# Optimization experiments

Measured on AMD Instinct MI355X. Metric: run time of the kernel, lower is better.

The kernel has to match this reference:

```python
import jax, jax.numpy as jnp
import numpy as np

N = 60000      # total atoms
E = 120000     # total directed bond edges
B = 1024       # molecules per batch
DIN = 88       # unpacked node feature bits
DE = 32        # unpacked edge feature bits
EMB = 256      # graph_dims
L = 4          # num MPNN layers
HID = 512      # attention hid_dim
H = 8          # n_heads
HD = HID // H  # head dim


def _bn(x, g, b):
    # BatchNorm1d in training mode: biased batch stats over dim 0
    m = x.mean(0)
    v = x.var(0)
    return g * (x - m) * jax.lax.rsqrt(v + 1e-5) + b


def setup_inputs() -> dict:
    ks = jax.random.split(jax.random.key(0), 24)
    p = lambda i, s: jax.random.normal(ks[i], s, jnp.float32) * 0.02
    z = lambda s: jnp.zeros(s, jnp.float32)
    o = lambda s: jnp.ones(s, jnp.float32)
    return {
        "x": jax.random.uniform(ks[0], (N, DIN), jnp.float32),
        "edge_index": jax.random.randint(ks[1], (2, E), 0, N),
        "edge_attr": jax.random.uniform(ks[2], (E, DE), jnp.float32),
        "batch": jnp.sort(jax.random.randint(ks[3], (N,), 0, B)),
        "fp": jax.random.uniform(ks[4], (B, 2048), jnp.float32),
        "target": (jax.random.uniform(ks[5], (B, 3)) > 0.5).astype(jnp.float32),
        "lin_w": p(6, (DIN, EMB)), "lin_b": z(EMB),
        "msg_w1": p(7, (L, 2 * EMB + DE, EMB)), "msg_b1": z((L, EMB)), "msg_g1": o((L, EMB)), "msg_be1": z((L, EMB)),
        "msg_w2": p(8, (L, EMB, EMB)), "msg_b2": z((L, EMB)), "msg_g2": o((L, EMB)), "msg_be2": z((L, EMB)),
        "upd_w1": p(9, (L, 2 * EMB, EMB)), "upd_b1": z((L, EMB)), "upd_g1": o((L, EMB)), "upd_be1": z((L, EMB)),
        "upd_w2": p(10, (L, EMB, EMB)), "upd_b2": z((L, EMB)), "upd_g2": o((L, EMB)), "upd_be2": z((L, EMB)),
        "gl_w1": p(11, (EMB, 1024)), "gl_b1": z(1024),
        "gl_w2": p(12, (1024, 1024)), "gl_b2": z(1024),
        "gl_w3": p(13, (1024, HID)), "gl_b3": z(HID),
        "fp_w": p(14, (2048, HID)), "fp_b": z(HID),
        "att_w": p(15, (2, 4, HID, HID)), "att_b": z((2, 4, HID)),
        "bind_w": p(16, (HID, 3)), "bind_b": z(3),
    }


def reference(x, edge_index, edge_attr, batch, fp, target,
              lin_w, lin_b,
              msg_w1, msg_b1, msg_g1, msg_be1, msg_w2, msg_b2, msg_g2, msg_be2,
              upd_w1, upd_b1, upd_g1, upd_be1, upd_w2, upd_b2, upd_g2, upd_be2,
              gl_w1, gl_b1, gl_w2, gl_b2, gl_w3, gl_b3,
              fp_w, fp_b, att_w, att_b, bind_w, bind_b):
    relu = jax.nn.relu
    src, dst = edge_index[0], edge_index[1]  # PyG: row 0 = source j, row 1 = target i
    h = x @ lin_w + lin_b  # (n, EMB)
    for l in range(msg_w1.shape[0]):
        # message: gather dst/src node feats + edge feats -> 2-layer BN MLP
        m = jnp.concatenate([h[dst], h[src], edge_attr], axis=-1)  # (e, 2*EMB+DE)
        m = relu(_bn(m @ msg_w1[l] + msg_b1[l], msg_g1[l], msg_be1[l]))
        m = relu(_bn(m @ msg_w2[l] + msg_b2[l], msg_g2[l], msg_be2[l]))
        # aggregate: scatter-add into destination nodes
        aggr = jax.ops.segment_sum(m, dst, num_segments=h.shape[0])  # (n, EMB)
        # update: concat with h -> 2-layer BN MLP; residual from MPNNModel
        u = jnp.concatenate([h, aggr], axis=-1)
        u = relu(_bn(u @ upd_w1[l] + upd_b1[l], upd_g1[l], upd_be1[l]))
        u = relu(_bn(u @ upd_w2[l] + upd_b2[l], upd_g2[l], upd_be2[l]))
        h = h + u
    # global mean pool per graph
    nb = fp.shape[0]
    sums = jax.ops.segment_sum(h, batch, num_segments=nb)
    cnt = jax.ops.segment_sum(jnp.ones((h.shape[0],), h.dtype), batch, num_segments=nb)
    g = sums / jnp.maximum(cnt, 1.0)[:, None]  # (B, EMB)
    # graph MLP (dropout = identity at inference)
    g = relu(g @ gl_w1 + gl_b1)
    g = relu(g @ gl_w2 + gl_b2)
    g = g @ gl_w3 + gl_b3  # (B, 512)
    fpf = relu(fp @ fp_w + fp_b)  # (B, 512)

    def attn(i, q, k, v):
        Q = (q @ att_w[i, 0] + att_b[i, 0]).reshape(-1, H, HD)
        K = (k @ att_w[i, 1] + att_b[i, 1]).reshape(-1, H, HD)
        V = (v @ att_w[i, 2] + att_b[i, 2]).reshape(-1, H, HD)
        # energy[b,h,d,e] = Q[b,h,d]*K[b,h,e] / sqrt(HD): outer product per head
        energy = jnp.einsum('bhd,bhe->bhde', Q, K) / jnp.sqrt(jnp.float32(HD))
        a = jax.nn.softmax(energy, axis=-1)
        o = jnp.einsum('bhde,bhe->bhd', a, V)
        # torch permute(0,2,1,3).view: flatten in (head_dim, head) order
        o = o.transpose(0, 2, 1).reshape(-1, H * HD)
        return o @ att_w[i, 3] + att_b[i, 3]

    g = g + attn(0, fpf, g, g)   # cross attention fp -> graph
    g = attn(1, g, g, g)          # self attention
    bind = g @ bind_w + bind_b    # (B, 3)
    # stable BCE-with-logits, mean reduction
    loss = jnp.mean(jnp.maximum(bind, 0.0) - bind * target + jnp.log1p(jnp.exp(-jnp.abs(bind))))
    return loss, jax.nn.sigmoid(bind)
```

## Files before the change

kernel.cpp:

```cpp
#include <hip/hip_runtime.h>
#include <hip/hip_bf16.h>
#include <math.h>

typedef long long i64;
typedef __hip_bfloat16 bf16;
typedef __attribute__((ext_vector_type(8))) short bfx8;
typedef __attribute__((ext_vector_type(4))) float f32x4;

#define NATOMS 60000
#define NEDGES 120000
#define NB     1024
#define EMB    256
#define NL     4
#define HIDF   512
#define NH     8
#define HD     64

__device__ __forceinline__ void storeT(float* p, float v) { *p = v; }
__device__ __forceinline__ void storeT(bf16* p, float v) { *p = __float2bfloat16(v); }

__device__ __forceinline__ void gl_lds16(const void* g, void* l) {
  __builtin_amdgcn_global_load_lds((const __attribute__((address_space(1))) void*)g,
                                   (__attribute__((address_space(3))) void*)l, 16, 0, 0);
}

template<int MODE, typename TO>
__global__ __launch_bounds__(256, 2) void mgemm_k(
    const bf16* __restrict__ A, const bf16* __restrict__ A2,
    const int* __restrict__ gdst, const int* __restrict__ gsrc,
    const bf16* __restrict__ Wt,
    const float* __restrict__ bias, const float* __restrict__ resid,
    TO* __restrict__ C, float* __restrict__ stats,
    int M, int Kp, int N, int doRelu)
{
  __shared__ short As[128 * 64];
  __shared__ short Bs[128 * 64];
  __shared__ float sSum[128], sSq[128];

  const int tid = threadIdx.x;
  const int w = tid >> 6, lane = tid & 63;
  const int wr = w >> 1, wc = w & 1;
  const int row0 = blockIdx.y * 128, col0 = blockIdx.x * 128;

  int rI[4], slotG[4], dIdx[4], sIdx[4], rClamp[4];
  #pragma unroll
  for (int i = 0; i < 4; ++i) {
    int lin = i * 256 + tid;
    int r = lin >> 3, sl = lin & 7;
    rI[i] = r;
    slotG[i] = sl ^ (r & 7);
    rClamp[i] = min(row0 + r, M - 1);
    if (MODE == 1) { dIdx[i] = gdst[rClamp[i]]; sIdx[i] = gsrc[rClamp[i]]; }
  }

  f32x4 acc[4][4];
  #pragma unroll
  for (int a = 0; a < 4; ++a)
    #pragma unroll
    for (int b = 0; b < 4; ++b)
      acc[a][b] = (f32x4){0.f, 0.f, 0.f, 0.f};

  const int KT = Kp >> 6;
  for (int kt = 0; kt < KT; ++kt) {
    const int k0 = kt << 6;
    #pragma unroll
    for (int i = 0; i < 4; ++i) {
      const bf16* g;
      int ko = slotG[i] * 8;
      if constexpr (MODE == 0) {
        g = A + (i64)rClamp[i] * Kp + k0 + ko;
      } else if constexpr (MODE == 1) {
        if (k0 < 256)      g = A  + (i64)dIdx[i] * EMB + k0 + ko;
        else if (k0 < 512) g = A  + (i64)sIdx[i] * EMB + (k0 - 256) + ko;
        else               g = A2 + (i64)rClamp[i] * 64 + (k0 - 512) + ko;
      } else {
        g = (k0 < 256) ? A  + (i64)rClamp[i] * EMB + k0 + ko
                       : A2 + (i64)rClamp[i] * EMB + (k0 - 256) + ko;
      }
      gl_lds16(g, (char*)&As[0] + i * 4096 + w * 1024);
    }
    #pragma unroll
    for (int i = 0; i < 4; ++i) {
      const bf16* g = Wt + (i64)(col0 + rI[i]) * Kp + k0 + slotG[i] * 8;
      gl_lds16(g, (char*)&Bs[0] + i * 4096 + w * 1024);
    }
    __syncthreads();

    #pragma unroll
    for (int ks = 0; ks < 2; ++ks) {
      bfx8 af[4], bf_[4];
      #pragma unroll
      for (int mi = 0; mi < 4; ++mi) {
        int r = wr * 64 + mi * 16 + (lane & 15);
        int q = ks * 4 + (lane >> 4);
        int s = q ^ (r & 7);
        af[mi] = *(const bfx8*)&As[r * 64 + s * 8];
      }
      #pragma unroll
      for (int ni = 0; ni < 4; ++ni) {
        int n = wc * 64 + ni * 16 + (lane & 15);
        int q = ks * 4 + (lane >> 4);
        int s = q ^ (n & 7);
        bf_[ni] = *(const bfx8*)&Bs[n * 64 + s * 8];
      }
      #pragma unroll
      for (int mi = 0; mi < 4; ++mi)
        #pragma unroll
        for (int ni = 0; ni < 4; ++ni)
          acc[mi][ni] = __builtin_amdgcn_mfma_f32_16x16x32_bf16(af[mi], bf_[ni], acc[mi][ni], 0, 0, 0);
    }
    __syncthreads();
  }

  #pragma unroll
  for (int mi = 0; mi < 4; ++mi) {
    #pragma unroll
    for (int j = 0; j < 4; ++j) {
      int row = row0 + wr * 64 + mi * 16 + (lane >> 4) * 4 + j;
      if (row < M) {
        #pragma unroll
        for (int ni = 0; ni < 4; ++ni) {
          int col = col0 + wc * 64 + ni * 16 + (lane & 15);
          float v = acc[mi][ni][j];
          if (bias)  v += bias[col];
          if (resid) v += resid[(i64)row * N + col];
          if (doRelu) v = fmaxf(v, 0.f);
          storeT(&C[(i64)row * N + col], v);
        }
      }
    }
  }

  if (stats) {
    if (tid < 128) { sSum[tid] = 0.f; sSq[tid] = 0.f; }
    __syncthreads();
    #pragma unroll
    for (int ni = 0; ni < 4; ++ni) {
      float ps = 0.f, pq = 0.f;
      #pragma unroll
      for (int mi = 0; mi < 4; ++mi)
        #pragma unroll
        for (int j = 0; j < 4; ++j) {
          int row = row0 + wr * 64 + mi * 16 + (lane >> 4) * 4 + j;
          if (row < M) { float v = acc[mi][ni][j]; ps += v; pq += v * v; }
        }
      ps += __shfl_xor(ps, 16); ps += __shfl_xor(ps, 32);
      pq += __shfl_xor(pq, 16); pq += __shfl_xor(pq, 32);
      if (lane < 16) {
        int c = wc * 64 + ni * 16 + lane;
        atomicAdd(&sSum[c], ps); atomicAdd(&sSq[c], pq);
      }
    }
    __syncthreads();
    if (tid < 128) {
      atomicAdd(&stats[col0 + tid], sSum[tid]);
      atomicAdd(&stats[256 + col0 + tid], sSq[tid]);
    }
  }
}

struct WDesc { const float* W; bf16* Wt; int K, N, Kp, bStart; };
struct WPack { WDesc d[29]; int cnt; };

__global__ __launch_bounds__(256) void wcvt_k(WPack p) {
  int bid = blockIdx.x;
  int di = 0;
  for (int i = 1; i < 29; ++i) if (i < p.cnt && bid >= p.d[i].bStart) di = i;
  WDesc wd = p.d[di];
  int t = bid - wd.bStart;
  int tilesN = wd.N >> 5;
  int tn = t % tilesN, tk = t / tilesN;
  __shared__ float tl[32][33];
  int tx = threadIdx.x & 31, ty = threadIdx.x >> 5;
  #pragma unroll
  for (int ii = 0; ii < 4; ++ii) {
    int k = tk * 32 + ty + ii * 8;
    int n = tn * 32 + tx;
    tl[ty + ii * 8][tx] = (k < wd.K) ? wd.W[(i64)k * wd.N + n] : 0.f;
  }
  __syncthreads();
  #pragma unroll
  for (int ii = 0; ii < 4; ++ii) {
    int n = tn * 32 + ty + ii * 8;
    int k = tk * 32 + tx;
    wd.Wt[(i64)n * wd.Kp + k] = __float2bfloat16(tl[tx][ty + ii * 8]);
  }
}

__global__ void padcvt_k(const float* __restrict__ S, bf16* __restrict__ D,
                         int rows, int sc, int dc) {
  i64 total = (i64)rows * dc;
  for (i64 i = (i64)blockIdx.x * blockDim.x + threadIdx.x; i < total;
       i += (i64)gridDim.x * blockDim.x) {
    int r = (int)(i / dc), c = (int)(i % dc);
    D[i] = __float2bfloat16(c < sc ? S[(i64)r * sc + c] : 0.f);
  }
}

__global__ void cvt_k(const float* __restrict__ S, bf16* __restrict__ D, i64 total) {
  i64 i0 = ((i64)blockIdx.x * blockDim.x + threadIdx.x) * 4;
  i64 stride = (i64)gridDim.x * blockDim.x * 4;
  for (i64 i = i0; i < total; i += stride) {
    float4 v = *(const float4*)(S + i);
    D[i + 0] = __float2bfloat16(v.x);
    D[i + 1] = __float2bfloat16(v.y);
    D[i + 2] = __float2bfloat16(v.z);
    D[i + 3] = __float2bfloat16(v.w);
  }
}

template<int HASADD>
__global__ __launch_bounds__(256) void bnap_k(
    const bf16* __restrict__ X, const bf16* __restrict__ addIn, bf16* __restrict__ Y,
    const float* __restrict__ st, const float* __restrict__ gam, const float* __restrict__ bet,
    i64 total, float invM)
{
  __shared__ float sc[256], sh[256];
  {
    int c = threadIdx.x;
    float mean = st[c] * invM;
    float var  = st[256 + c] * invM - mean * mean;
    float rs   = rsqrtf(var + 1e-5f);
    float s    = gam[c] * rs;
    sc[c] = s; sh[c] = bet[c] - mean * s;
  }
  __syncthreads();
  i64 i0 = ((i64)blockIdx.x * blockDim.x + threadIdx.x) * 8;
  i64 stride = (i64)gridDim.x * blockDim.x * 8;
  for (i64 i = i0; i < total; i += stride) {
    bfx8 xv = *(const bfx8*)((const short*)X + i);
    bfx8 av;
    if (HASADD) av = *(const bfx8*)((const short*)addIn + i);
    int c0 = (int)(i & 255);
    bfx8 o;
    #pragma unroll
    for (int j = 0; j < 8; ++j) {
      unsigned short u = (unsigned short)xv[j];
      float x = __bfloat162float(*reinterpret_cast<const bf16*>(&u));
      int c = c0 + j;
      float t = fmaxf(x * sc[c] + sh[c], 0.f);
      if (HASADD) {
        unsigned short ua = (unsigned short)av[j];
        t += __bfloat162float(*reinterpret_cast<const bf16*>(&ua));
      }
      bf16 b = __float2bfloat16(t);
      o[j] = (short)*reinterpret_cast<unsigned short*>(&b);
    }
    *(bfx8*)((short*)Y + i) = o;
  }
}

__global__ void scatter_k(const bf16* __restrict__ m, const int* __restrict__ dst,
                          float* __restrict__ aggr, i64 total) {
  i64 i0 = (i64)blockIdx.x * blockDim.x + threadIdx.x;
  i64 stride = (i64)gridDim.x * blockDim.x;
  for (i64 i = i0; i < total; i += stride) {
    int e = (int)(i >> 8);
    int c = (int)(i & 255);
    atomicAdd(&aggr[(i64)dst[e] * EMB + c], __bfloat162float(m[i]));
  }
}

__global__ __launch_bounds__(256) void pool_seg_k(const bf16* __restrict__ h,
                                                  const int* __restrict__ batch,
                                                  bf16* __restrict__ g0b) {
  int b = blockIdx.x, c = threadIdx.x;
  int lo = 0, hi = NATOMS;
  while (lo < hi) { int mid = (lo + hi) >> 1; if (batch[mid] < b) lo = mid + 1; else hi = mid; }
  int s = lo;
  hi = NATOMS;
  while (lo < hi) { int mid = (lo + hi) >> 1; if (batch[mid] < b + 1) lo = mid + 1; else hi = mid; }
  int e = lo;
  float acc = 0.f;
  for (int r = s; r < e; ++r) acc += __bfloat162float(h[(i64)r * EMB + c]);
  g0b[b * EMB + c] = __float2bfloat16(acc / (float)max(e - s, 1));
}

__global__ __launch_bounds__(64) void attn_k(const float* __restrict__ Q, const float* __restrict__ K,
                                             const float* __restrict__ V, bf16* __restrict__ O) {
  int b = blockIdx.x >> 3, hh = blockIdx.x & 7;
  int d = threadIdx.x;
  __shared__ float Ks[HD], Vs[HD];
  Ks[d] = K[(i64)b * HIDF + hh * HD + d];
  Vs[d] = V[(i64)b * HIDF + hh * HD + d];
  __syncthreads();
  float q = Q[(i64)b * HIDF + hh * HD + d] * 0.125f;
  float mx = -1e30f;
  #pragma unroll
  for (int e = 0; e < HD; ++e) mx = fmaxf(mx, q * Ks[e]);
  float s = 0.f, o = 0.f;
  #pragma unroll
  for (int e = 0; e < HD; ++e) {
    float p = expf(q * Ks[e] - mx);
    s += p; o += p * Vs[e];
  }
  O[(i64)b * HIDF + d * NH + hh] = __float2bfloat16(o / s);
}

__global__ __launch_bounds__(256) void bind_loss_k(const float* __restrict__ g, const float* __restrict__ W,
                                                   const float* __restrict__ bb, const float* __restrict__ tgt,
                                                   float* __restrict__ out) {
  int tid = threadIdx.x;
  float lsum = 0.f;
  for (int r = tid; r < NB; r += 256) {
    float a0 = bb[0], a1 = bb[1], a2 = bb[2];
    const float* gr = g + (i64)r * HIDF;
    for (int k = 0; k < HIDF; ++k) {
      float gv = gr[k];
      a0 += gv * W[k * 3 + 0];
      a1 += gv * W[k * 3 + 1];
      a2 += gv * W[k * 3 + 2];
    }
    float bv[3] = {a0, a1, a2};
    #pragma unroll
    for (int j = 0; j < 3; ++j) {
      float xv = bv[j], t = tgt[r * 3 + j];
      lsum += fmaxf(xv, 0.f) - xv * t + log1pf(expf(-fabsf(xv)));
      out[1 + r * 3 + j] = 1.f / (1.f + expf(-xv));
    }
  }
  __shared__ float red[256];
  red[tid] = lsum;
  __syncthreads();
  for (int s = 128; s > 0; s >>= 1) {
    if (tid < s) red[tid] += red[tid + s];
    __syncthreads();
  }
  if (tid == 0) out[0] = red[0] / (float)(NB * 3);
}

extern "C" void kernel_launch(void* const* d_in, const int* in_sizes, int n_in,
                              void* d_out, int out_size, void* d_ws, size_t ws_size,
                              hipStream_t stream) {
  const float* x         = (const float*)d_in[0];
  const int*   ei        = (const int*)  d_in[1];
  const float* edge_attr = (const float*)d_in[2];
  const int*   batch     = (const int*)  d_in[3];
  const float* fp        = (const float*)d_in[4];
  const float* target    = (const float*)d_in[5];
  const float* lin_w     = (const float*)d_in[6];
  const float* lin_b     = (const float*)d_in[7];
  const float* msg_w1    = (const float*)d_in[8];
  const float* msg_g1    = (const float*)d_in[10];
  const float* msg_be1   = (const float*)d_in[11];
  const float* msg_w2    = (const float*)d_in[12];
  const float* msg_g2    = (const float*)d_in[14];
  const float* msg_be2   = (const float*)d_in[15];
  const float* upd_w1    = (const float*)d_in[16];
  const float* upd_g1    = (const float*)d_in[18];
  const float* upd_be1   = (const float*)d_in[19];
  const float* upd_w2    = (const float*)d_in[20];
  const float* upd_g2    = (const float*)d_in[22];
  const float* upd_be2   = (const float*)d_in[23];
  const float* gl_w1     = (const float*)d_in[24];
  const float* gl_b1     = (const float*)d_in[25];
  const float* gl_w2     = (const float*)d_in[26];
  const float* gl_b2     = (const float*)d_in[27];
  const float* gl_w3     = (const float*)d_in[28];
  const float* gl_b3     = (const float*)d_in[29];
  const float* fp_w      = (const float*)d_in[30];
  const float* fp_b      = (const float*)d_in[31];
  const float* att_w     = (const float*)d_in[32];
  const float* att_b     = (const float*)d_in[33];
  const float* bind_w    = (const float*)d_in[34];
  const float* bind_b    = (const float*)d_in[35];

  const int* src = ei;
  const int* dst = ei + NEDGES;

  char* base = (char*)d_ws;
  float* stats = (float*)base;
  char* p = base + 8192 * 4;
  bf16* h_bf  = (bf16*)p; p += (i64)NATOMS * EMB * 2;
  bf16* ea_bf = (bf16*)p; p += (i64)NEDGES * 64 * 2;
  bf16* wt    = (bf16*)p; p += 6651904LL * 2;
  char* R1 = p; p += 61440000LL;
  char* R2 = p;

  bf16* Wt_lin = wt; wt += 256 * 128;
  bf16 *Wt_m1[NL], *Wt_m2[NL], *Wt_u1[NL], *Wt_u2[NL];
  for (int l = 0; l < NL; ++l) { Wt_m1[l] = wt; wt += 256 * 576; }
  for (int l = 0; l < NL; ++l) { Wt_m2[l] = wt; wt += 256 * 256; }
  for (int l = 0; l < NL; ++l) { Wt_u1[l] = wt; wt += 256 * 512; }
  for (int l = 0; l < NL; ++l) { Wt_u2[l] = wt; wt += 256 * 256; }
  bf16* Wt_gl1 = wt; wt += 1024 * 256;
  bf16* Wt_gl2 = wt; wt += 1024 * 1024;
  bf16* Wt_gl3 = wt; wt += 512 * 1024;
  bf16* Wt_fp  = wt; wt += 512 * 2048;
  bf16* Wt_att[8];
  for (int i = 0; i < 8; ++i) { Wt_att[i] = wt; wt += 512 * 512; }

  bf16*  x_bf  = (bf16*)R2;
  bf16*  m1b   = (bf16*)R1;
  bf16*  m2b   = (bf16*)R2;
  float* aggr  = (float*)R1;
  bf16*  aggrb = (bf16*)R2;
  bf16*  u1b   = (bf16*)(R2 + (i64)NATOMS * EMB * 2);
  bf16*  u2b   = (bf16*)R1;

  bf16*  g0b  = (bf16*)R1;
  bf16*  gh1b = g0b + (i64)NB * EMB;
  bf16*  gh2b = gh1b + (i64)NB * 1024;
  float* g3   = (float*)(gh2b + (i64)NB * 1024);
  bf16*  g3b  = (bf16*)(g3 + (i64)NB * HIDF);
  bf16*  fpb  = g3b + (i64)NB * HIDF;
  bf16*  fpfb = fpb + (i64)NB * 2048;
  float* Qb   = (float*)(fpfb + (i64)NB * HIDF);
  float* Kb   = Qb + (i64)NB * HIDF;
  float* Vb   = Kb + (i64)NB * HIDF;
  bf16*  Obb  = (bf16*)(Vb + (i64)NB * HIDF);
  float* gc1  = (float*)(Obb + (i64)NB * HIDF);
  bf16*  gc1b = (bf16*)(gc1 + (i64)NB * HIDF);
  float* gc2  = (float*)(gc1b + (i64)NB * HIDF);

  hipMemsetAsync(stats, 0, 8192 * 4, stream);

  WPack pk; int bs = 0, di = 0;
  auto addW = [&](const float* Wp, bf16* Wtp, int K, int N, int Kp) {
    pk.d[di].W = Wp; pk.d[di].Wt = Wtp; pk.d[di].K = K; pk.d[di].N = N;
    pk.d[di].Kp = Kp; pk.d[di].bStart = bs;
    bs += (Kp / 32) * (N / 32); ++di;
  };
  addW(lin_w, Wt_lin, 88, 256, 128);
  for (int l = 0; l < NL; ++l) addW(msg_w1 + (i64)l * 544 * 256, Wt_m1[l], 544, 256, 576);
  for (int l = 0; l < NL; ++l) addW(msg_w2 + (i64)l * 256 * 256, Wt_m2[l], 256, 256, 256);
  for (int l = 0; l < NL; ++l) addW(upd_w1 + (i64)l * 512 * 256, Wt_u1[l], 512, 256, 512);
  for (int l = 0; l < NL; ++l) addW(upd_w2 + (i64)l * 256 * 256, Wt_u2[l], 256, 256, 256);
  addW(gl_w1, Wt_gl1, 256, 1024, 256);
  addW(gl_w2, Wt_gl2, 1024, 1024, 1024);
  addW(gl_w3, Wt_gl3, 1024, 512, 1024);
  addW(fp_w, Wt_fp, 2048, 512, 2048);
  for (int i = 0; i < 8; ++i) addW(att_w + (i64)i * 512 * 512, Wt_att[i], 512, 512, 512);
  pk.cnt = di;
  wcvt_k<<<bs, 256, 0, stream>>>(pk);

  padcvt_k<<<2048, 256, 0, stream>>>(x, x_bf, NATOMS, 88, 128);
  padcvt_k<<<2048, 256, 0, stream>>>(edge_attr, ea_bf, NEDGES, 32, 64);

  dim3 gE(2, (NEDGES + 127) / 128), gN(2, (NATOMS + 127) / 128);

  mgemm_k<0, bf16><<<gN, 256, 0, stream>>>(x_bf, nullptr, nullptr, nullptr, Wt_lin,
      lin_b, nullptr, h_bf, nullptr, NATOMS, 128, 256, 0);

  for (int l = 0; l < NL; ++l) {
    float* st0 = stats + (l * 4 + 0) * 512;
    float* st1 = stats + (l * 4 + 1) * 512;
    float* st2 = stats + (l * 4 + 2) * 512;
    float* st3 = stats + (l * 4 + 3) * 512;
    mgemm_k<1, bf16><<<gE, 256, 0, stream>>>(h_bf, ea_bf, dst, src, Wt_m1[l],
        nullptr, nullptr, m1b, st0, NEDGES, 576, 256, 0);
    bnap_k<0><<<2048, 256, 0, stream>>>(m1b, nullptr, m1b, st0,
        msg_g1 + l * EMB, msg_be1 + l * EMB, (i64)NEDGES * EMB, 1.f / NEDGES);
    mgemm_k<0, bf16><<<gE, 256, 0, stream>>>(m1b, nullptr, nullptr, nullptr, Wt_m2[l],
        nullptr, nullptr, m2b, st1, NEDGES, 256, 256, 0);
    bnap_k<0><<<2048, 256, 0, stream>>>(m2b, nullptr, m2b, st1,
        msg_g2 + l * EMB, msg_be2 + l * EMB, (i64)NEDGES * EMB, 1.f / NEDGES);
    hipMemsetAsync(aggr, 0, (size_t)NATOMS * EMB * 4, stream);
    scatter_k<<<4096, 256, 0, stream>>>(m2b, dst, aggr, (i64)NEDGES * EMB);
    cvt_k<<<2048, 256, 0, stream>>>(aggr, aggrb, (i64)NATOMS * EMB);
    mgemm_k<2, bf16><<<gN, 256, 0, stream>>>(h_bf, aggrb, nullptr, nullptr, Wt_u1[l],
        nullptr, nullptr, u1b, st2, NATOMS, 512, 256, 0);
    bnap_k<0><<<2048, 256, 0, stream>>>(u1b, nullptr, u1b, st2,
        upd_g1 + l * EMB, upd_be1 + l * EMB, (i64)NATOMS * EMB, 1.f / NATOMS);
    mgemm_k<0, bf16><<<gN, 256, 0, stream>>>(u1b, nullptr, nullptr, nullptr, Wt_u2[l],
        nullptr, nullptr, u2b, st3, NATOMS, 256, 256, 0);
    bnap_k<1><<<2048, 256, 0, stream>>>(u2b, h_bf, h_bf, st3,
        upd_g2 + l * EMB, upd_be2 + l * EMB, (i64)NATOMS * EMB, 1.f / NATOMS);
  }

  pool_seg_k<<<NB, 256, 0, stream>>>(h_bf, batch, g0b);

  mgemm_k<0, bf16><<<dim3(8, 8), 256, 0, stream>>>(g0b, nullptr, nullptr, nullptr, Wt_gl1,
      gl_b1, nullptr, gh1b, nullptr, NB, 256, 1024, 1);
  mgemm_k<0, bf16><<<dim3(8, 8), 256, 0, stream>>>(gh1b, nullptr, nullptr, nullptr, Wt_gl2,
      gl_b2, nullptr, gh2b, nullptr, NB, 1024, 1024, 1);
  mgemm_k<0, float><<<dim3(4, 8), 256, 0, stream>>>(gh2b, nullptr, nullptr, nullptr, Wt_gl3,
      gl_b3, nullptr, g3, nullptr, NB, 1024, 512, 0);
  cvt_k<<<512, 256, 0, stream>>>(g3, g3b, (i64)NB * HIDF);
  cvt_k<<<512, 256, 0, stream>>>(fp, fpb, (i64)NB * 2048);
  mgemm_k<0, bf16><<<dim3(4, 8), 256, 0, stream>>>(fpb, nullptr, nullptr, nullptr, Wt_fp,
      fp_b, nullptr, fpfb, nullptr, NB, 2048, 512, 1);

  mgemm_k<0, float><<<dim3(4, 8), 256, 0, stream>>>(fpfb, nullptr, nullptr, nullptr, Wt_att[0],
      att_b + 0 * HIDF, nullptr, Qb, nullptr, NB, 512, 512, 0);
  mgemm_k<0, float><<<dim3(4, 8), 256, 0, stream>>>(g3b, nullptr, nullptr, nullptr, Wt_att[1],
      att_b + 1 * HIDF, nullptr, Kb, nullptr, NB, 512, 512, 0);
  mgemm_k<0, float><<<dim3(4, 8), 256, 0, stream>>>(g3b, nullptr, nullptr, nullptr, Wt_att[2],
      att_b + 2 * HIDF, nullptr, Vb, nullptr, NB, 512, 512, 0);
  attn_k<<<NB * NH, 64, 0, stream>>>(Qb, Kb, Vb, Obb);
  mgemm_k<0, float><<<dim3(4, 8), 256, 0, stream>>>(Obb, nullptr, nullptr, nullptr, Wt_att[3],
      att_b + 3 * HIDF, g3, gc1, nullptr, NB, 512, 512, 0);
  cvt_k<<<512, 256, 0, stream>>>(gc1, gc1b, (i64)NB * HIDF);

  mgemm_k<0, float><<<dim3(4, 8), 256, 0, stream>>>(gc1b, nullptr, nullptr, nullptr, Wt_att[4],
      att_b + 4 * HIDF, nullptr, Qb, nullptr, NB, 512, 512, 0);
  mgemm_k<0, float><<<dim3(4, 8), 256, 0, stream>>>(gc1b, nullptr, nullptr, nullptr, Wt_att[5],
      att_b + 5 * HIDF, nullptr, Kb, nullptr, NB, 512, 512, 0);
  mgemm_k<0, float><<<dim3(4, 8), 256, 0, stream>>>(gc1b, nullptr, nullptr, nullptr, Wt_att[6],
      att_b + 6 * HIDF, nullptr, Vb, nullptr, NB, 512, 512, 0);
  attn_k<<<NB * NH, 64, 0, stream>>>(Qb, Kb, Vb, Obb);
  mgemm_k<0, float><<<dim3(4, 8), 256, 0, stream>>>(Obb, nullptr, nullptr, nullptr, Wt_att[7],
      att_b + 7 * HIDF, nullptr, gc2, nullptr, NB, 512, 512, 0);

  bind_loss_k<<<1, 256, 0, stream>>>(gc2, bind_w, bind_b, target, (float*)d_out);
}
```

Baseline: 2.182 ms.

## Replace atomic scatter-add with CSR gather fused with message batchnorm

```diff
diff --git a/kernel.cpp b/kernel.cpp
--- a/kernel.cpp
+++ b/kernel.cpp
@@ -250,14 +250,67 @@
   }
 }
 
-__global__ void scatter_k(const bf16* __restrict__ m, const int* __restrict__ dst,
-                          float* __restrict__ aggr, i64 total) {
-  i64 i0 = (i64)blockIdx.x * blockDim.x + threadIdx.x;
-  i64 stride = (i64)gridDim.x * blockDim.x;
-  for (i64 i = i0; i < total; i += stride) {
-    int e = (int)(i >> 8);
-    int c = (int)(i & 255);
-    atomicAdd(&aggr[(i64)dst[e] * EMB + c], __bfloat162float(m[i]));
+__global__ void deg_k(const int* __restrict__ dst, int* __restrict__ deg) {
+  int e = blockIdx.x * blockDim.x + threadIdx.x;
+  if (e < NEDGES) atomicAdd(&deg[dst[e]], 1);
+}
+
+__global__ __launch_bounds__(1024) void scan_k(const int* __restrict__ deg,
+                                               int* __restrict__ starts,
+                                               int* __restrict__ cursor) {
+  __shared__ int sh[1024];
+  __shared__ int roff;
+  if (threadIdx.x == 0) roff = 0;
+  __syncthreads();
+  const int nch = (NATOMS + 1023) / 1024;
+  for (int ch = 0; ch < nch; ++ch) {
+    int i = ch * 1024 + threadIdx.x;
+    int v = (i < NATOMS) ? deg[i] : 0;
+    sh[threadIdx.x] = v;
+    __syncthreads();
+    for (int ofs = 1; ofs < 1024; ofs <<= 1) {
+      int t = (threadIdx.x >= ofs) ? sh[threadIdx.x - ofs] : 0;
+      __syncthreads();
+      sh[threadIdx.x] += t;
+      __syncthreads();
+    }
+    int incl = sh[threadIdx.x];
+    int base = roff;
+    if (i < NATOMS) { int st = base + incl - v; starts[i] = st; cursor[i] = st; }
+    __syncthreads();
+    if (threadIdx.x == 1023) roff = base + sh[1023];
+    __syncthreads();
+  }
+  if (threadIdx.x == 0) starts[NATOMS] = NEDGES;
+}
+
+__global__ void fill_k(const int* __restrict__ dst, int* __restrict__ cursor,
+                       int* __restrict__ elist) {
+  int e = blockIdx.x * blockDim.x + threadIdx.x;
+  if (e < NEDGES) { int pos = atomicAdd(&cursor[dst[e]], 1); elist[pos] = e; }
+}
+
+__global__ __launch_bounds__(256) void gather_k(
+    const bf16* __restrict__ m2, const int* __restrict__ starts,
+    const int* __restrict__ elist,
+    const float* __restrict__ st, const float* __restrict__ gam,
+    const float* __restrict__ bet, float invM, bf16* __restrict__ aggrb)
+{
+  const int c = threadIdx.x;
+  float mean = st[c] * invM;
+  float var  = st[256 + c] * invM - mean * mean;
+  float rs   = rsqrtf(var + 1e-5f);
+  float scv  = gam[c] * rs;
+  float shv  = bet[c] - mean * scv;
+  for (int n = blockIdx.x; n < NATOMS; n += gridDim.x) {
+    int s = starts[n], e = starts[n + 1];
+    float acc = 0.f;
+    for (int i = s; i < e; ++i) {
+      int eid = elist[i];
+      float v = __bfloat162float(m2[(i64)eid * EMB + c]);
+      acc += fmaxf(v * scv + shv, 0.f);
+    }
+    aggrb[(i64)n * EMB + c] = __float2bfloat16(acc);
   }
 }
 
@@ -371,6 +424,10 @@
   char* base = (char*)d_ws;
   float* stats = (float*)base;
   char* p = base + 8192 * 4;
+  int* deg    = (int*)p; p += 60000 * 4;
+  int* starts = (int*)p; p += 60004 * 4;
+  int* cursor = (int*)p; p += 60000 * 4;
+  int* elist  = (int*)p; p += 120000 * 4;
   bf16* h_bf  = (bf16*)p; p += (i64)NATOMS * EMB * 2;
   bf16* ea_bf = (bf16*)p; p += (i64)NEDGES * 64 * 2;
   bf16* wt    = (bf16*)p; p += 6651904LL * 2;
@@ -393,9 +450,8 @@
   bf16*  x_bf  = (bf16*)R2;
   bf16*  m1b   = (bf16*)R1;
   bf16*  m2b   = (bf16*)R2;
-  float* aggr  = (float*)R1;
-  bf16*  aggrb = (bf16*)R2;
-  bf16*  u1b   = (bf16*)(R2 + (i64)NATOMS * EMB * 2);
+  bf16*  aggrb = (bf16*)R1;
+  bf16*  u1b   = (bf16*)R2;
   bf16*  u2b   = (bf16*)R1;
 
   bf16*  g0b  = (bf16*)R1;
@@ -413,7 +469,11 @@
   bf16*  gc1b = (bf16*)(gc1 + (i64)NB * HIDF);
   float* gc2  = (float*)(gc1b + (i64)NB * HIDF);
 
-  hipMemsetAsync(stats, 0, 8192 * 4, stream);
+  hipMemsetAsync(stats, 0, (8192 + 60000) * 4, stream);
+
+  deg_k<<<(NEDGES + 255) / 256, 256, 0, stream>>>(dst, deg);
+  scan_k<<<1, 1024, 0, stream>>>(deg, starts, cursor);
+  fill_k<<<(NEDGES + 255) / 256, 256, 0, stream>>>(dst, cursor, elist);
 
   WPack pk; int bs = 0, di = 0;
   auto addW = [&](const float* Wp, bf16* Wtp, int K, int N, int Kp) {
@@ -453,11 +513,8 @@
         msg_g1 + l * EMB, msg_be1 + l * EMB, (i64)NEDGES * EMB, 1.f / NEDGES);
     mgemm_k<0, bf16><<<gE, 256, 0, stream>>>(m1b, nullptr, nullptr, nullptr, Wt_m2[l],
         nullptr, nullptr, m2b, st1, NEDGES, 256, 256, 0);
-    bnap_k<0><<<2048, 256, 0, stream>>>(m2b, nullptr, m2b, st1,
-        msg_g2 + l * EMB, msg_be2 + l * EMB, (i64)NEDGES * EMB, 1.f / NEDGES);
-    hipMemsetAsync(aggr, 0, (size_t)NATOMS * EMB * 4, stream);
-    scatter_k<<<4096, 256, 0, stream>>>(m2b, dst, aggr, (i64)NEDGES * EMB);
-    cvt_k<<<2048, 256, 0, stream>>>(aggr, aggrb, (i64)NATOMS * EMB);
+    gather_k<<<2048, 256, 0, stream>>>(m2b, starts, elist, st1,
+        msg_g2 + l * EMB, msg_be2 + l * EMB, 1.f / NEDGES, aggrb);
     mgemm_k<2, bf16><<<gN, 256, 0, stream>>>(h_bf, aggrb, nullptr, nullptr, Wt_u1[l],
         nullptr, nullptr, u1b, st2, NATOMS, 512, 256, 0);
     bnap_k<0><<<2048, 256, 0, stream>>>(u1b, nullptr, u1b, st2,
```

After: 2.041 ms. -6.5%, faster.
